# Kernel tuning notes

Measured on AMD Instinct MI355X. Metric: run time of the kernel, lower is better.

## Reference

```python
import jax, jax.numpy as jnp
import numpy as np
import math

B, S, N_UNITS, D_K = 8, 2048, 1024, 512


def setup_inputs() -> dict:
    key = jax.random.key(0)
    ks = jax.random.split(key, 8)
    scale = 1.0 / math.sqrt(N_UNITS)
    query = jax.random.normal(ks[0], (B, S, N_UNITS), dtype=jnp.float32)
    k_in = jax.random.normal(ks[1], (B, S, N_UNITS), dtype=jnp.float32)
    v_in = jax.random.normal(ks[2], (B, S, N_UNITS), dtype=jnp.float32)
    # custom multiplicative mask: causal lower-triangular, broadcast over batch
    mask = jnp.broadcast_to(jnp.tril(jnp.ones((S, S), dtype=jnp.float32)), (B, S, S))
    Wq = jax.random.normal(ks[3], (N_UNITS, D_K), dtype=jnp.float32) * scale
    Wk = jax.random.normal(ks[4], (N_UNITS, D_K), dtype=jnp.float32) * scale
    Wv = jax.random.normal(ks[5], (N_UNITS, D_K), dtype=jnp.float32) * scale
    bq = jnp.zeros((D_K,), dtype=jnp.float32)
    bk = jnp.zeros((D_K,), dtype=jnp.float32)
    bv = jnp.zeros((D_K,), dtype=jnp.float32)
    return {"query": query, "key": k_in, "value": v_in, "mask": mask,
            "Wq": Wq, "bq": bq, "Wk": Wk, "bk": bk, "Wv": Wv, "bv": bv}


def reference(query, key, value, mask, Wq, bq, Wk, bk, Wv, bv):
    d_k = Wq.shape[-1]
    Q = jnp.einsum('bsn,nd->bsd', query, Wq) + bq  # [B,S,Dk]
    K = jnp.einsum('bsn,nd->bsd', key, Wk) + bk
    V = jnp.einsum('bsn,nd->bsd', value, Wv) + bv
    # scores [B,S,S]
    x_hat = jnp.einsum('bqd,bkd->bqk', Q, K) / jnp.sqrt(jnp.float32(d_k))
    # custom multiplicative mask: x*mask - 1e9*(1-mask)
    x_hat_masked = x_hat * mask - 1e9 * (1.0 - mask)
    attn = jax.nn.softmax(x_hat_masked, axis=-1)
    # dropout = 0.0 (eval mode) -> identity
    out = jnp.einsum('bqk,bkd->bqd', attn, V)
    return out
```

## Files before the change

### kernel.cpp

```cpp
#include <hip/hip_runtime.h>

typedef __bf16 bf16_t;
typedef __attribute__((ext_vector_type(4))) __bf16 bf16x4;
typedef __attribute__((ext_vector_type(8))) __bf16 bf16x8;
typedef __attribute__((ext_vector_type(4))) float f32x4;

#define B_    8
#define S_    2048
#define NU    1024
#define DK    512
#define MROWS (B_ * S_)
#define PBATCH (128 * 128 * 136)

#define WAITVM(N) asm volatile("s_waitcnt vmcnt(" #N ")" ::: "memory")
#define WAITLG    asm volatile("s_waitcnt lgkmcnt(0)" ::: "memory")
#define BAR       asm volatile("s_barrier" ::: "memory")

__device__ __forceinline__ f32x4 mfma16(bf16x8 a, bf16x8 b, f32x4 c) {
  return __builtin_amdgcn_mfma_f32_16x16x32_bf16(a, b, c, 0, 0, 0);
}

__device__ __forceinline__ void async_load16(const void* g, void* l) {
  __builtin_amdgcn_global_load_lds(
      (const __attribute__((address_space(1))) unsigned int*)g,
      (__attribute__((address_space(3))) unsigned int*)l, 16, 0, 0);
}

__device__ __forceinline__ bf16x8 cvt8(f32x4 x0, f32x4 x1) {
  bf16x8 r;
#pragma unroll
  for (int j = 0; j < 4; ++j) { r[j] = (bf16_t)x0[j]; r[j + 4] = (bf16_t)x1[j]; }
  return r;
}

__device__ __forceinline__ void stage_tile(const bf16_t* __restrict__ src,
                                           int rstride, bf16_t* dst, int k0,
                                           int tid) {
#pragma unroll
  for (int j = 0; j < 2; ++j) {
    const int g = j * 256 + tid;
    const int ln = g >> 3, c = g & 7;
    const int cs = c ^ (ln & 7);
    const int srow = 2 * ln + (cs >> 2);
    async_load16(src + (size_t)srow * rstride + k0 + (cs & 3) * 8, dst + g * 8);
  }
}

__device__ __forceinline__ void stage_tile64(const bf16_t* __restrict__ src,
                                             int rstride, bf16_t* dst, int k0,
                                             int tid) {
  const int ln = tid >> 3, c = tid & 7;
  const int cs = c ^ (ln & 7);
  const int srow = 2 * ln + (cs >> 2);
  async_load16(src + (size_t)srow * rstride + k0 + (cs & 3) * 8, dst + tid * 8);
}

__device__ __forceinline__ void stage_tile_f32(const float* __restrict__ src,
                                               int rstride, float* dst, int k0,
                                               int tid) {
#pragma unroll
  for (int j = 0; j < 4; ++j) {
    const int g = j * 256 + tid;
    const int row = g >> 3, c = g & 7;
    const int cs = c ^ (row & 7);
    async_load16(src + (size_t)row * rstride + k0 + (cs << 2), dst + g * 4);
  }
}

__device__ __forceinline__ bf16x8 frag(const bf16_t* buf, int row, int q) {
  const int ln = row >> 1;
  const int cp = (((row & 1) << 2) | q) ^ (ln & 7);
  return *(const bf16x8*)(buf + ln * 64 + cp * 8);
}

__device__ __forceinline__ bf16x8 frag_f32(const float* buf, int row, int q) {
  const int s = row & 7;
  const f32x4 x0 = *(const f32x4*)&buf[row * 32 + (((q * 2)) ^ s) * 4];
  const f32x4 x1 = *(const f32x4*)&buf[row * 32 + (((q * 2) | 1) ^ s) * 4];
  return cvt8(x0, x1);
}

__global__ __launch_bounds__(256) void transpose_w_kernel(
    const float* __restrict__ Wq, const float* __restrict__ Wk,
    const float* __restrict__ Wv, bf16_t* __restrict__ Wt) {
  const float* W = (blockIdx.z == 0) ? Wq : (blockIdx.z == 1) ? Wk : Wv;
  bf16_t* Wo = Wt + (size_t)blockIdx.z * DK * NU;
  __shared__ float tile[32][33];
  const int t = threadIdx.x;
  const int r = t >> 5, c = t & 31;
  const int kbase = blockIdx.y * 32, nbase = blockIdx.x * 32;
#pragma unroll
  for (int i = 0; i < 4; ++i)
    tile[r + i * 8][c] = W[(size_t)(kbase + r + i * 8) * DK + nbase + c];
  __syncthreads();
#pragma unroll
  for (int i = 0; i < 4; ++i)
    Wo[(size_t)(nbase + r + i * 8) * NU + kbase + c] = (bf16_t)tile[c][r + i * 8];
}

__global__ __launch_bounds__(256, 3) void xw3_gemm_kernel(
    const float* __restrict__ q_in, const float* __restrict__ k_in,
    const float* __restrict__ v_in, const bf16_t* __restrict__ Wt,
    const float* __restrict__ bq, const float* __restrict__ bk,
    const float* __restrict__ bv, bf16_t* __restrict__ Qo,
    bf16_t* __restrict__ Ko, bf16_t* __restrict__ Vt) {
  const int bx = blockIdx.x;
  const int z = bx >> 9;
  const int t = bx & 511;
  const int g = t >> 5, nt = (t >> 3) & 3, r8 = t & 7;
  const int mt = g * 8 + r8;
  const int m0 = mt * 128;
  const int n0 = nt * 128;
  const float* X = (z == 0) ? q_in : (z == 1) ? k_in : v_in;
  const float* bias = (z == 0) ? bq : (z == 1) ? bk : bv;

  const int tid = threadIdx.x;
  const int wave = tid >> 6, lane = tid & 63;
  const int l16 = lane & 15, quad = lane >> 4;
  const int wm = (wave >> 1) * 64, wn = (wave & 1) * 64;

  __shared__ __align__(16) unsigned char smem[49152];
  float* ldsA = (float*)smem;
  bf16_t* ldsB = (bf16_t*)(smem + 32768);

  const float* Ag = X + (size_t)m0 * NU;
  const bf16_t* Bg = Wt + (size_t)z * DK * NU + (size_t)n0 * NU;

  f32x4 acc[4][4] = {};

  stage_tile_f32(Ag, NU, ldsA, 0, tid);
  stage_tile(Bg, NU, ldsB, 0, tid);
  const int NS = 32;
  for (int ks = 0; ks < NS; ++ks) {
    WAITVM(0);
    BAR;
    if (ks + 1 < NS) {
      stage_tile_f32(Ag, NU, ldsA + ((ks + 1) & 1) * 4096, (ks + 1) * 32, tid);
      stage_tile(Bg, NU, ldsB + ((ks + 1) & 1) * 4096, (ks + 1) * 32, tid);
    }
    const float* ac = ldsA + (ks & 1) * 4096;
    const bf16_t* bc = ldsB + (ks & 1) * 4096;
    bf16x8 af[4], bfr[4];
#pragma unroll
    for (int i = 0; i < 4; ++i) af[i] = frag_f32(ac, wm + i * 16 + l16, quad);
#pragma unroll
    for (int j = 0; j < 4; ++j) bfr[j] = frag(bc, wn + j * 16 + l16, quad);
#pragma unroll
    for (int i = 0; i < 4; ++i)
#pragma unroll
      for (int j = 0; j < 4; ++j)
        acc[i][j] = mfma16(af[i], bfr[j], acc[i][j]);
  }

  if (z != 2) {
    bf16_t* Out = (z == 0) ? Qo : Ko;
#pragma unroll
    for (int j = 0; j < 4; ++j) {
      const int cn = n0 + wn + j * 16 + l16;
      const float bz = bias[cn];
#pragma unroll
      for (int i = 0; i < 4; ++i) {
        const int rm = m0 + wm + i * 16 + quad * 4;
#pragma unroll
        for (int r = 0; r < 4; ++r)
          Out[(size_t)(rm + r) * DK + cn] = (bf16_t)(acc[i][j][r] + bz);
      }
    }
  } else {
    bf16_t* Ts = (bf16_t*)smem;
    BAR;
#pragma unroll
    for (int j = 0; j < 4; ++j) {
      const int cnl = wn + j * 16 + l16;
      const float bz = bias[n0 + cnl];
#pragma unroll
      for (int i = 0; i < 4; ++i) {
        const int rs = wm + i * 16 + quad * 4;
        bf16x4 tv;
#pragma unroll
        for (int r = 0; r < 4; ++r) tv[r] = (bf16_t)(acc[i][j][r] + bz);
        *(bf16x4*)&Ts[cnl * 136 + rs] = tv;
      }
    }
    WAITLG; BAR;
    const int bb2 = m0 >> 11, sl = m0 & 2047;
    const int row = tid >> 1, half = tid & 1;
    bf16_t* dst = Vt + ((size_t)bb2 * DK + n0 + row) * S_ + sl + half * 64;
    const bf16_t* sp = &Ts[row * 136 + half * 64];
#pragma unroll
    for (int k = 0; k < 8; ++k)
      *(bf16x8*)(dst + k * 8) = *(const bf16x8*)(sp + k * 8);
  }
}

__global__ __launch_bounds__(256, 4) void qk_p_kernel(
    const bf16_t* __restrict__ Q, const bf16_t* __restrict__ K,
    bf16_t* __restrict__ P, float* __restrict__ Lp) {
  const int bx = blockIdx.x;
  const int b = bx & 7;
  const int t = bx >> 3;
  int mt = 0;
  while (((mt + 1) * (mt + 2)) / 2 <= t) ++mt;
  const int nt = t - (mt * (mt + 1)) / 2;
  const int klen = (mt + 1) * 128;

  const int tid = threadIdx.x;
  const int wave = tid >> 6, lane = tid & 63;
  const int l16 = lane & 15, quad = lane >> 4;
  const int wm = (wave >> 1) * 64, wn = (wave & 1) * 64;

  __shared__ __align__(16) unsigned char smem[32768];
  bf16_t* ldsA = (bf16_t*)smem;
  bf16_t* ldsB = (bf16_t*)(smem + 16384);

  const bf16_t* Ag = Q + (size_t)(b * S_ + mt * 128) * DK;
  const bf16_t* Bg = K + (size_t)(b * S_ + nt * 128) * DK;

  f32x4 acc[4][4] = {};

  stage_tile(Ag, DK, ldsA, 0, tid);
  stage_tile(Bg, DK, ldsB, 0, tid);
  const int NS = 16;
  for (int ks = 0; ks < NS; ++ks) {
    WAITVM(0);
    BAR;
    if (ks + 1 < NS) {
      stage_tile(Ag, DK, ldsA + ((ks + 1) & 1) * 4096, (ks + 1) * 32, tid);
      stage_tile(Bg, DK, ldsB + ((ks + 1) & 1) * 4096, (ks + 1) * 32, tid);
    }
    const bf16_t* ac = ldsA + (ks & 1) * 4096;
    const bf16_t* bc = ldsB + (ks & 1) * 4096;
    bf16x8 af[4], bfr[4];
#pragma unroll
    for (int i = 0; i < 4; ++i) af[i] = frag(ac, wm + i * 16 + l16, quad);
#pragma unroll
    for (int j = 0; j < 4; ++j) bfr[j] = frag(bc, wn + j * 16 + l16, quad);
#pragma unroll
    for (int i = 0; i < 4; ++i)
#pragma unroll
      for (int j = 0; j < 4; ++j)
        acc[i][j] = mfma16(af[i], bfr[j], acc[i][j]);
  }

  const float scale = 0.04419417382415922f;
  bf16_t* Pt = P + (size_t)b * PBATCH + (size_t)8192 * mt * (mt + 1);
  float* Lph = Lp + ((size_t)(b * 136 + t) * 2 + (wn >> 6)) * 128;
#pragma unroll
  for (int i = 0; i < 4; ++i) {
#pragma unroll
    for (int r = 0; r < 4; ++r) {
      const int lrow = wm + i * 16 + quad * 4 + r;
      const int srow = mt * 128 + lrow;
      float rsum = 0.f;
#pragma unroll
      for (int j = 0; j < 4; ++j) {
        const int scol = nt * 128 + wn + j * 16 + l16;
        const float p =
            (scol > srow) ? 0.f : __expf(acc[i][j][r] * scale - 10.0f);
        rsum += p;
        Pt[(size_t)lrow * klen + scol] = (bf16_t)p;
      }
#pragma unroll
      for (int off = 8; off >= 1; off >>= 1)
        rsum += __shfl_xor(rsum, off, 64);
      if (l16 == 0) Lph[lrow] = rsum;
    }
  }
}

__global__ __launch_bounds__(256, 4) void pv_kernel(
    const bf16_t* __restrict__ P, const bf16_t* __restrict__ Vt,
    const float* __restrict__ Lp, float* __restrict__ Out) {
  const int bx = blockIdx.x;
  const int low = bx & 63;
  const int b = low & 7;
  const int d0 = ((low >> 3) & 3) * 128;
  const int half = (low >> 5) & 1;
  const int g = bx >> 6;
  const int q2 = g >> 2, rb = g & 3;
  const int mt = (q2 == 0) ? 15 - 2 * rb
               : (q2 == 1) ? 2 * rb
               : (q2 == 2) ? 14 - 2 * rb
                           : 1 + 2 * rb;
  const int klen = (mt + 1) * 128;
  const int NS = (mt + 1) * 4;

  const int tid = threadIdx.x;
  const int wave = tid >> 6, lane = tid & 63;
  const int l16 = lane & 15, quad = lane >> 4;
  const int wm = (wave >> 1) * 32, wn = (wave & 1) * 64;

  __shared__ __align__(16) unsigned char smem[24832];
  bf16_t* ldsA = (bf16_t*)smem;
  bf16_t* ldsB = (bf16_t*)(smem + 8192);
  float* Ls = (float*)(smem + 24576);

  const bf16_t* Ag = P + (size_t)b * PBATCH + (size_t)8192 * mt * (mt + 1) +
                     (size_t)(half * 64) * klen;
  const bf16_t* Bg = Vt + ((size_t)b * DK + d0) * S_;

  f32x4 acc[2][4] = {};

  stage_tile64(Ag, klen, ldsA, 0, tid);
  stage_tile(Bg, S_, ldsB, 0, tid);
  for (int ks = 0; ks < NS; ++ks) {
    WAITVM(0);
    BAR;
    if (ks + 1 < NS) {
      stage_tile64(Ag, klen, ldsA + ((ks + 1) & 1) * 2048, (ks + 1) * 32, tid);
      stage_tile(Bg, S_, ldsB + ((ks + 1) & 1) * 4096, (ks + 1) * 32, tid);
    }
    const bf16_t* ac = ldsA + (ks & 1) * 2048;
    const bf16_t* bc = ldsB + (ks & 1) * 4096;
    bf16x8 af[2], bfr[4];
#pragma unroll
    for (int i = 0; i < 2; ++i) af[i] = frag(ac, wm + i * 16 + l16, quad);
#pragma unroll
    for (int j = 0; j < 4; ++j) bfr[j] = frag(bc, wn + j * 16 + l16, quad);
#pragma unroll
    for (int i = 0; i < 2; ++i)
#pragma unroll
      for (int j = 0; j < 4; ++j)
        acc[i][j] = mfma16(af[i], bfr[j], acc[i][j]);
  }

  if (tid < 64) {
    const int rowit = half * 64 + tid;
    const float* lp =
        Lp + ((size_t)(b * 136 + (mt * (mt + 1)) / 2) * 2) * 128 + rowit;
    float s = 0.f;
    for (int n = 0; n <= mt; ++n) s += lp[n * 256] + lp[n * 256 + 128];
    Ls[tid] = s;
  }
  WAITLG; BAR;

  const int m0 = b * S_ + mt * 128 + half * 64;
#pragma unroll
  for (int i = 0; i < 2; ++i) {
#pragma unroll
    for (int r = 0; r < 4; ++r) {
      const int lr = wm + i * 16 + quad * 4 + r;
      const float inv = 1.0f / Ls[lr];
      float* orow = Out + (size_t)(m0 + lr) * DK + d0;
#pragma unroll
      for (int j = 0; j < 4; ++j)
        orow[wn + j * 16 + l16] = acc[i][j][r] * inv;
    }
  }
}

extern "C" void kernel_launch(void* const* d_in, const int* in_sizes, int n_in,
                              void* d_out, int out_size, void* d_ws, size_t ws_size,
                              hipStream_t stream) {
  const float* query = (const float*)d_in[0];
  const float* key_i = (const float*)d_in[1];
  const float* value = (const float*)d_in[2];
  const float* Wq = (const float*)d_in[4];
  const float* bq = (const float*)d_in[5];
  const float* Wk = (const float*)d_in[6];
  const float* bk = (const float*)d_in[7];
  const float* Wv = (const float*)d_in[8];
  const float* bv = (const float*)d_in[9];
  float* out = (float*)d_out;

  bf16_t* Wt = (bf16_t*)d_ws;
  bf16_t* Qw = Wt + (size_t)3 * DK * NU;
  bf16_t* Kw = Qw + (size_t)MROWS * DK;
  bf16_t* Vw = Kw + (size_t)MROWS * DK;
  bf16_t* Pw = Vw + (size_t)MROWS * DK;
  float* Lpw = (float*)(Pw + (size_t)B_ * PBATCH);

  transpose_w_kernel<<<dim3(16, 32, 3), 256, 0, stream>>>(Wq, Wk, Wv, Wt);
  xw3_gemm_kernel<<<1536, 256, 0, stream>>>(query, key_i, value, Wt, bq, bk,
                                            bv, Qw, Kw, Vw);
  qk_p_kernel<<<1088, 256, 0, stream>>>(Qw, Kw, Pw, Lpw);
  pv_kernel<<<1024, 256, 0, stream>>>(Pw, Vw, Lpw, out);
}
```

Before: 442.6 us.

## Deepen GEMM pipelines to four K-stages with two-step iterations and setprio

All three GEMM kernels move from double buffering with one K-step per iteration to a four-stage LDS ring, processed two K-steps per iteration. Fragments are read into registers before the barrier, the next loads are issued, and the MFMAs run under raised wave priority. The projection GEMM now loads its fp32 activations through registers and converts them to bf16 once before writing LDS, which halves the A-tile LDS footprint and removes the per-fragment conversion. The block index mapping becomes plain row-major. The extra LDS lowers the occupancy hints (3→2, 4→2, 4→3), trading parallelism for more latency hiding.

Result: faster. 420.9 us (median of 2 runs) (-4.9%).

```diff
diff --git a/kernel.cpp b/kernel.cpp
--- a/kernel.cpp
+++ b/kernel.cpp
@@ -55,29 +55,10 @@
   async_load16(src + (size_t)srow * rstride + k0 + (cs & 3) * 8, dst + tid * 8);
 }
 
-__device__ __forceinline__ void stage_tile_f32(const float* __restrict__ src,
-                                               int rstride, float* dst, int k0,
-                                               int tid) {
-#pragma unroll
-  for (int j = 0; j < 4; ++j) {
-    const int g = j * 256 + tid;
-    const int row = g >> 3, c = g & 7;
-    const int cs = c ^ (row & 7);
-    async_load16(src + (size_t)row * rstride + k0 + (cs << 2), dst + g * 4);
-  }
-}
-
 __device__ __forceinline__ bf16x8 frag(const bf16_t* buf, int row, int q) {
   const int ln = row >> 1;
   const int cp = (((row & 1) << 2) | q) ^ (ln & 7);
   return *(const bf16x8*)(buf + ln * 64 + cp * 8);
-}
-
-__device__ __forceinline__ bf16x8 frag_f32(const float* buf, int row, int q) {
-  const int s = row & 7;
-  const f32x4 x0 = *(const f32x4*)&buf[row * 32 + (((q * 2)) ^ s) * 4];
-  const f32x4 x1 = *(const f32x4*)&buf[row * 32 + (((q * 2) | 1) ^ s) * 4];
-  return cvt8(x0, x1);
 }
 
 __global__ __launch_bounds__(256) void transpose_w_kernel(
@@ -98,7 +79,7 @@
     Wo[(size_t)(nbase + r + i * 8) * NU + kbase + c] = (bf16_t)tile[c][r + i * 8];
 }
 
-__global__ __launch_bounds__(256, 3) void xw3_gemm_kernel(
+__global__ __launch_bounds__(256, 2) void xw3_gemm_kernel(
     const float* __restrict__ q_in, const float* __restrict__ k_in,
     const float* __restrict__ v_in, const bf16_t* __restrict__ Wt,
     const float* __restrict__ bq, const float* __restrict__ bk,
@@ -107,10 +88,8 @@
   const int bx = blockIdx.x;
   const int z = bx >> 9;
   const int t = bx & 511;
-  const int g = t >> 5, nt = (t >> 3) & 3, r8 = t & 7;
-  const int mt = g * 8 + r8;
-  const int m0 = mt * 128;
-  const int n0 = nt * 128;
+  const int m0 = (t & 127) * 128;
+  const int n0 = (t >> 7) * 128;
   const float* X = (z == 0) ? q_in : (z == 1) ? k_in : v_in;
   const float* bias = (z == 0) ? bq : (z == 1) ? bk : bv;
 
@@ -119,37 +98,97 @@
   const int l16 = lane & 15, quad = lane >> 4;
   const int wm = (wave >> 1) * 64, wn = (wave & 1) * 64;
 
-  __shared__ __align__(16) unsigned char smem[49152];
-  float* ldsA = (float*)smem;
+  __shared__ __align__(16) unsigned char smem[65536];
+  bf16_t* ldsA = (bf16_t*)smem;
   bf16_t* ldsB = (bf16_t*)(smem + 32768);
 
   const float* Ag = X + (size_t)m0 * NU;
   const bf16_t* Bg = Wt + (size_t)z * DK * NU + (size_t)n0 * NU;
 
+  int g0 = 2 * tid, g1 = 2 * tid + 1;
+  const int cs0 = (g0 & 7) ^ ((g0 >> 3) & 7);
+  const int cs1 = (g1 & 7) ^ ((g1 >> 3) & 7);
+  const int sr0 = 2 * (g0 >> 3) + (cs0 >> 2), c40 = cs0 & 3;
+  const int sr1 = 2 * (g1 >> 3) + (cs1 >> 2), c41 = cs1 & 3;
+  const float* ap0 = Ag + (size_t)sr0 * NU + c40 * 8;
+  const float* ap1 = Ag + (size_t)sr1 * NU + c41 * 8;
+
+#define XW_A_LOAD(S, K0)                                                      \
+  f32x4 xl##S##0 = *(const f32x4*)(ap0 + (K0));                               \
+  f32x4 xl##S##1 = *(const f32x4*)(ap0 + (K0) + 4);                           \
+  f32x4 xl##S##2 = *(const f32x4*)(ap1 + (K0));                               \
+  f32x4 xl##S##3 = *(const f32x4*)(ap1 + (K0) + 4);
+#define XW_A_WRITE(S, BUFE)                                                   \
+  *(bf16x8*)&ldsA[(BUFE) + g0 * 8] = cvt8(xl##S##0, xl##S##1);                \
+  *(bf16x8*)&ldsA[(BUFE) + g1 * 8] = cvt8(xl##S##2, xl##S##3);
+
   f32x4 acc[4][4] = {};
 
-  stage_tile_f32(Ag, NU, ldsA, 0, tid);
-  stage_tile(Bg, NU, ldsB, 0, tid);
+  {
+    XW_A_LOAD(0, 0)
+    XW_A_LOAD(1, 32)
+    XW_A_LOAD(2, 64)
+    XW_A_LOAD(3, 96)
+    stage_tile(Bg, NU, ldsB, 0, tid);
+    stage_tile(Bg, NU, ldsB + 4096, 32, tid);
+    stage_tile(Bg, NU, ldsB + 8192, 64, tid);
+    stage_tile(Bg, NU, ldsB + 12288, 96, tid);
+    XW_A_WRITE(0, 0)
+    XW_A_WRITE(1, 4096)
+    XW_A_WRITE(2, 8192)
+    XW_A_WRITE(3, 12288)
+    WAITVM(0);
+    WAITLG;
+    BAR;
+  }
+
   const int NS = 32;
-  for (int ks = 0; ks < NS; ++ks) {
-    WAITVM(0);
-    BAR;
-    if (ks + 1 < NS) {
-      stage_tile_f32(Ag, NU, ldsA + ((ks + 1) & 1) * 4096, (ks + 1) * 32, tid);
-      stage_tile(Bg, NU, ldsB + ((ks + 1) & 1) * 4096, (ks + 1) * 32, tid);
-    }
-    const float* ac = ldsA + (ks & 1) * 4096;
-    const bf16_t* bc = ldsB + (ks & 1) * 4096;
-    bf16x8 af[4], bfr[4];
-#pragma unroll
-    for (int i = 0; i < 4; ++i) af[i] = frag_f32(ac, wm + i * 16 + l16, quad);
-#pragma unroll
-    for (int j = 0; j < 4; ++j) bfr[j] = frag(bc, wn + j * 16 + l16, quad);
-#pragma unroll
-    for (int i = 0; i < 4; ++i)
-#pragma unroll
-      for (int j = 0; j < 4; ++j)
-        acc[i][j] = mfma16(af[i], bfr[j], acc[i][j]);
+  for (int j = 0; j < NS / 2; ++j) {
+    const int ks2 = 2 * j;
+    const int base = (j & 1) * 8192;
+    bf16x8 af[2][4], bfr[2][4];
+#pragma unroll
+    for (int s = 0; s < 2; ++s)
+#pragma unroll
+      for (int i = 0; i < 4; ++i) {
+        af[s][i] = frag(ldsA + base + s * 4096, wm + i * 16 + l16, quad);
+        bfr[s][i] = frag(ldsB + base + s * 4096, wn + i * 16 + l16, quad);
+      }
+    WAITLG;
+    BAR;
+    const bool more = (ks2 + 4) < NS;
+    if (more) {
+      const int k4 = (ks2 + 4) * 32;
+      XW_A_LOAD(4, k4)
+      XW_A_LOAD(5, k4 + 32)
+      stage_tile(Bg, NU, ldsB + base, k4, tid);
+      stage_tile(Bg, NU, ldsB + base + 4096, k4 + 32, tid);
+      __builtin_amdgcn_s_setprio(1);
+#pragma unroll
+      for (int s = 0; s < 2; ++s)
+#pragma unroll
+        for (int i = 0; i < 4; ++i)
+#pragma unroll
+          for (int jj = 0; jj < 4; ++jj)
+            acc[i][jj] = mfma16(af[s][i], bfr[s][jj], acc[i][jj]);
+      __builtin_amdgcn_s_setprio(0);
+      WAITVM(4);
+      XW_A_WRITE(4, base)
+      XW_A_WRITE(5, base + 4096)
+    } else {
+      __builtin_amdgcn_s_setprio(1);
+#pragma unroll
+      for (int s = 0; s < 2; ++s)
+#pragma unroll
+        for (int i = 0; i < 4; ++i)
+#pragma unroll
+          for (int jj = 0; jj < 4; ++jj)
+            acc[i][jj] = mfma16(af[s][i], bfr[s][jj], acc[i][jj]);
+      __builtin_amdgcn_s_setprio(0);
+      WAITVM(0);
+    }
+    WAITLG;
+    BAR;
   }
 
   if (z != 2) {
@@ -191,9 +230,11 @@
     for (int k = 0; k < 8; ++k)
       *(bf16x8*)(dst + k * 8) = *(const bf16x8*)(sp + k * 8);
   }
-}
-
-__global__ __launch_bounds__(256, 4) void qk_p_kernel(
+#undef XW_A_LOAD
+#undef XW_A_WRITE
+}
+
+__global__ __launch_bounds__(256, 2) void qk_p_kernel(
     const bf16_t* __restrict__ Q, const bf16_t* __restrict__ K,
     bf16_t* __restrict__ P, float* __restrict__ Lp) {
   const int bx = blockIdx.x;
@@ -209,9 +250,9 @@
   const int l16 = lane & 15, quad = lane >> 4;
   const int wm = (wave >> 1) * 64, wn = (wave & 1) * 64;
 
-  __shared__ __align__(16) unsigned char smem[32768];
+  __shared__ __align__(16) unsigned char smem[65536];
   bf16_t* ldsA = (bf16_t*)smem;
-  bf16_t* ldsB = (bf16_t*)(smem + 16384);
+  bf16_t* ldsB = (bf16_t*)(smem + 32768);
 
   const bf16_t* Ag = Q + (size_t)(b * S_ + mt * 128) * DK;
   const bf16_t* Bg = K + (size_t)(b * S_ + nt * 128) * DK;
@@ -220,26 +261,48 @@
 
   stage_tile(Ag, DK, ldsA, 0, tid);
   stage_tile(Bg, DK, ldsB, 0, tid);
+  stage_tile(Ag, DK, ldsA + 4096, 32, tid);
+  stage_tile(Bg, DK, ldsB + 4096, 32, tid);
+  stage_tile(Ag, DK, ldsA + 8192, 64, tid);
+  stage_tile(Bg, DK, ldsB + 8192, 64, tid);
+  stage_tile(Ag, DK, ldsA + 12288, 96, tid);
+  stage_tile(Bg, DK, ldsB + 12288, 96, tid);
+  WAITVM(8);
+  BAR;
+
   const int NS = 16;
-  for (int ks = 0; ks < NS; ++ks) {
-    WAITVM(0);
-    BAR;
-    if (ks + 1 < NS) {
-      stage_tile(Ag, DK, ldsA + ((ks + 1) & 1) * 4096, (ks + 1) * 32, tid);
-      stage_tile(Bg, DK, ldsB + ((ks + 1) & 1) * 4096, (ks + 1) * 32, tid);
-    }
-    const bf16_t* ac = ldsA + (ks & 1) * 4096;
-    const bf16_t* bc = ldsB + (ks & 1) * 4096;
-    bf16x8 af[4], bfr[4];
-#pragma unroll
-    for (int i = 0; i < 4; ++i) af[i] = frag(ac, wm + i * 16 + l16, quad);
-#pragma unroll
-    for (int j = 0; j < 4; ++j) bfr[j] = frag(bc, wn + j * 16 + l16, quad);
-#pragma unroll
-    for (int i = 0; i < 4; ++i)
-#pragma unroll
-      for (int j = 0; j < 4; ++j)
-        acc[i][j] = mfma16(af[i], bfr[j], acc[i][j]);
+  for (int j = 0; j < NS / 2; ++j) {
+    const int ks2 = 2 * j;
+    const int base = (j & 1) * 8192;
+    bf16x8 af[2][4], bfr[2][4];
+#pragma unroll
+    for (int s = 0; s < 2; ++s)
+#pragma unroll
+      for (int i = 0; i < 4; ++i) {
+        af[s][i] = frag(ldsA + base + s * 4096, wm + i * 16 + l16, quad);
+        bfr[s][i] = frag(ldsB + base + s * 4096, wn + i * 16 + l16, quad);
+      }
+    WAITLG;
+    BAR;
+    const bool more = (ks2 + 4) < NS;
+    if (more) {
+      const int k4 = (ks2 + 4) * 32;
+      stage_tile(Ag, DK, ldsA + base, k4, tid);
+      stage_tile(Bg, DK, ldsB + base, k4, tid);
+      stage_tile(Ag, DK, ldsA + base + 4096, k4 + 32, tid);
+      stage_tile(Bg, DK, ldsB + base + 4096, k4 + 32, tid);
+    }
+    __builtin_amdgcn_s_setprio(1);
+#pragma unroll
+    for (int s = 0; s < 2; ++s)
+#pragma unroll
+      for (int i = 0; i < 4; ++i)
+#pragma unroll
+        for (int jj = 0; jj < 4; ++jj)
+          acc[i][jj] = mfma16(af[s][i], bfr[s][jj], acc[i][jj]);
+    __builtin_amdgcn_s_setprio(0);
+    if (more) { WAITVM(8); } else { WAITVM(0); }
+    BAR;
   }
 
   const float scale = 0.04419417382415922f;
@@ -268,7 +331,7 @@
   }
 }
 
-__global__ __launch_bounds__(256, 4) void pv_kernel(
+__global__ __launch_bounds__(256, 3) void pv_kernel(
     const bf16_t* __restrict__ P, const bf16_t* __restrict__ Vt,
     const float* __restrict__ Lp, float* __restrict__ Out) {
   const int bx = blockIdx.x;
@@ -290,10 +353,10 @@
   const int l16 = lane & 15, quad = lane >> 4;
   const int wm = (wave >> 1) * 32, wn = (wave & 1) * 64;
 
-  __shared__ __align__(16) unsigned char smem[24832];
+  __shared__ __align__(16) unsigned char smem[49664];
   bf16_t* ldsA = (bf16_t*)smem;
-  bf16_t* ldsB = (bf16_t*)(smem + 8192);
-  float* Ls = (float*)(smem + 24576);
+  bf16_t* ldsB = (bf16_t*)(smem + 16384);
+  float* Ls = (float*)(smem + 49152);
 
   const bf16_t* Ag = P + (size_t)b * PBATCH + (size_t)8192 * mt * (mt + 1) +
                      (size_t)(half * 64) * klen;
@@ -303,25 +366,50 @@
 
   stage_tile64(Ag, klen, ldsA, 0, tid);
   stage_tile(Bg, S_, ldsB, 0, tid);
-  for (int ks = 0; ks < NS; ++ks) {
-    WAITVM(0);
-    BAR;
-    if (ks + 1 < NS) {
-      stage_tile64(Ag, klen, ldsA + ((ks + 1) & 1) * 2048, (ks + 1) * 32, tid);
-      stage_tile(Bg, S_, ldsB + ((ks + 1) & 1) * 4096, (ks + 1) * 32, tid);
-    }
-    const bf16_t* ac = ldsA + (ks & 1) * 2048;
-    const bf16_t* bc = ldsB + (ks & 1) * 4096;
-    bf16x8 af[2], bfr[4];
-#pragma unroll
-    for (int i = 0; i < 2; ++i) af[i] = frag(ac, wm + i * 16 + l16, quad);
-#pragma unroll
-    for (int j = 0; j < 4; ++j) bfr[j] = frag(bc, wn + j * 16 + l16, quad);
-#pragma unroll
-    for (int i = 0; i < 2; ++i)
-#pragma unroll
-      for (int j = 0; j < 4; ++j)
-        acc[i][j] = mfma16(af[i], bfr[j], acc[i][j]);
+  stage_tile64(Ag, klen, ldsA + 2048, 32, tid);
+  stage_tile(Bg, S_, ldsB + 4096, 32, tid);
+  stage_tile64(Ag, klen, ldsA + 4096, 64, tid);
+  stage_tile(Bg, S_, ldsB + 8192, 64, tid);
+  stage_tile64(Ag, klen, ldsA + 6144, 96, tid);
+  stage_tile(Bg, S_, ldsB + 12288, 96, tid);
+  WAITVM(6);
+  BAR;
+
+  for (int j = 0; j < NS / 2; ++j) {
+    const int ks2 = 2 * j;
+    const int baseA = (j & 1) * 4096;
+    const int baseB = (j & 1) * 8192;
+    bf16x8 af[2][2], bfr[2][4];
+#pragma unroll
+    for (int s = 0; s < 2; ++s) {
+#pragma unroll
+      for (int i = 0; i < 2; ++i)
+        af[s][i] = frag(ldsA + baseA + s * 2048, wm + i * 16 + l16, quad);
+#pragma unroll
+      for (int i = 0; i < 4; ++i)
+        bfr[s][i] = frag(ldsB + baseB + s * 4096, wn + i * 16 + l16, quad);
+    }
+    WAITLG;
+    BAR;
+    const bool more = (ks2 + 4) < NS;
+    if (more) {
+      const int k4 = (ks2 + 4) * 32;
+      stage_tile64(Ag, klen, ldsA + baseA, k4, tid);
+      stage_tile(Bg, S_, ldsB + baseB, k4, tid);
+      stage_tile64(Ag, klen, ldsA + baseA + 2048, k4 + 32, tid);
+      stage_tile(Bg, S_, ldsB + baseB + 4096, k4 + 32, tid);
+    }
+    __builtin_amdgcn_s_setprio(1);
+#pragma unroll
+    for (int s = 0; s < 2; ++s)
+#pragma unroll
+      for (int i = 0; i < 2; ++i)
+#pragma unroll
+        for (int jj = 0; jj < 4; ++jj)
+          acc[i][jj] = mfma16(af[s][i], bfr[s][jj], acc[i][jj]);
+    __builtin_amdgcn_s_setprio(0);
+    if (more) { WAITVM(6); } else { WAITVM(0); }
+    BAR;
   }
 
   if (tid < 64) {
```
